# Kernel tuning notes

Measured on AMD Instinct MI355X. Metric: run time of the kernel, lower is better.

## Reference

```python
import jax, jax.numpy as jnp
import numpy as np

N, C = 65536, 1000

def setup_inputs() -> dict:
    key = jax.random.key(0)
    k1, k2 = jax.random.split(key)
    inp = jax.random.normal(k1, (N, C), dtype=jnp.float32)
    tgt = jax.random.randint(k2, (N,), 0, C, dtype=jnp.int64)
    return {"input": inp, "target": tgt}

def reference(input, target):
    # sign mask: +1 at the target class, -1 elsewhere (replaces the scatter loop)
    one_hot = jnp.arange(input.shape[1])[None, :] == target[:, None]  # [N, C] bool
    m = jnp.where(one_hot, input, -input)
    # piecewise huber-hinge: if m >= -1 -> max(0, 1-m)^2 else -4*m
    hinge = jnp.maximum(0.0, 1.0 - m)
    loss = jnp.where(m >= -1.0, hinge * hinge, -4.0 * m)
    return jnp.sum(loss) / target.shape[0]
```

## Files before the change

kernel.cpp:

```cpp
#include <hip/hip_runtime.h>


typedef float f4 __attribute__((ext_vector_type(4)));

constexpr int N_ROWS = 65536;
constexpr int N_COLS = 1000;
constexpr int F4_PER_ROW = N_COLS / 4;
constexpr int TOTAL_F4 = N_ROWS * F4_PER_ROW;

constexpr int BLOCK = 256;
constexpr int MAIN_GRID = 2000;
constexpr int CORR_GRID = 64;
constexpr int STRIDE_F4 = MAIN_GRID * BLOCK;
constexpr int ITERS = TOTAL_F4 / STRIDE_F4;
constexpr int BATCH = 8;

__device__ __forceinline__ float huber_f(float h) {
    float hc = fmaxf(fminf(h, 2.0f), 0.0f);
    return hc * fmaf(h, 2.0f, -hc);
}

__global__ __launch_bounds__(BLOCK) void mhl_kernel(const f4* __restrict__ in,
                                                    const float* __restrict__ in_f,
                                                    const int* __restrict__ tgt,
                                                    float* __restrict__ out) {
    float acc = 0.0f;

    if (blockIdx.x < CORR_GRID) {
        int tid = blockIdx.x * BLOCK + threadIdx.x;
#pragma unroll
        for (int k = 0; k < 4; ++k) {
            int r = tid + k * (CORR_GRID * BLOCK);
            int t = tgt[r];
            float x = in_f[r * N_COLS + t];
            acc += huber_f(1.0f - x) - huber_f(1.0f + x);
        }
    } else {
        int idx = (blockIdx.x - CORR_GRID) * BLOCK + threadIdx.x;
        int p = idx;
#pragma unroll 1
        for (int it = 0; it < ITERS / BATCH; ++it) {
            f4 v[BATCH];
#pragma unroll
            for (int j = 0; j < BATCH; ++j)
                v[j] = in[p + j * STRIDE_F4];
#pragma unroll
            for (int j = 0; j < BATCH; ++j) {
#pragma unroll
                for (int e = 0; e < 4; ++e) {
                    float h = 1.0f + v[j][e];
                    float hc = fmaxf(fminf(h, 2.0f), 0.0f);
                    acc = fmaf(hc, fmaf(h, 2.0f, -hc), acc);
                }
            }
            p += BATCH * STRIDE_F4;
        }
    }

#pragma unroll
    for (int off = 32; off > 0; off >>= 1)
        acc += __shfl_down(acc, off, 64);

    __shared__ float wsum[BLOCK / 64];
    int wid = threadIdx.x >> 6;
    int lane = threadIdx.x & 63;
    if (lane == 0) wsum[wid] = acc;
    __syncthreads();

    if (threadIdx.x == 0) {
        float s = wsum[0] + wsum[1] + wsum[2] + wsum[3];
        atomicAdd(out, s * (1.0f / (float)N_ROWS));
    }
}

extern "C" void kernel_launch(void* const* d_in, const int* in_sizes, int n_in,
                              void* d_out, int out_size, void* d_ws, size_t ws_size,
                              hipStream_t stream) {
    const f4* in = (const f4*)d_in[0];
    const float* in_f = (const float*)d_in[0];
    const int* tgt = (const int*)d_in[1];
    float* out = (float*)d_out;

    (void)hipMemsetAsync(out, 0, sizeof(float), stream);

    mhl_kernel<<<MAIN_GRID + CORR_GRID, BLOCK, 0, stream>>>(in, in_f, tgt, out);
}
```

Measured before the change: 58.66 us.

## Fold target-correction into main blocks and replace atomics with two-pass reduction

Removes the separate correction blocks: each of the 2000 streaming blocks now also handles 33 rows' target-class correction using its first threads. The global atomicAdd plus memset is replaced by per-block partial sums written to workspace, followed by a single-block reduce kernel. This drops the memset launch and atomic contention, but adds a second kernel launch and a dependency on the workspace buffer.

New measurement: 47.40 us. 1.24x faster.

```diff
diff --git a/kernel.cpp b/kernel.cpp
--- a/kernel.cpp
+++ b/kernel.cpp
@@ -9,52 +9,49 @@
 constexpr int TOTAL_F4 = N_ROWS * F4_PER_ROW;
 
 constexpr int BLOCK = 256;
-constexpr int MAIN_GRID = 2000;
-constexpr int CORR_GRID = 64;
-constexpr int STRIDE_F4 = MAIN_GRID * BLOCK;
+constexpr int GRID = 2000;
+constexpr int STRIDE_F4 = GRID * BLOCK;
 constexpr int ITERS = TOTAL_F4 / STRIDE_F4;
 constexpr int BATCH = 8;
+constexpr int ROWS_PER_BLOCK = 33;
 
 __device__ __forceinline__ float huber_f(float h) {
     float hc = fmaxf(fminf(h, 2.0f), 0.0f);
     return hc * fmaf(h, 2.0f, -hc);
 }
 
-__global__ __launch_bounds__(BLOCK) void mhl_kernel(const f4* __restrict__ in,
-                                                    const float* __restrict__ in_f,
-                                                    const int* __restrict__ tgt,
-                                                    float* __restrict__ out) {
+__global__ __launch_bounds__(BLOCK) void mhl_main(const f4* __restrict__ in,
+                                                  const float* __restrict__ in_f,
+                                                  const int* __restrict__ tgt,
+                                                  float* __restrict__ partial) {
     float acc = 0.0f;
 
-    if (blockIdx.x < CORR_GRID) {
-        int tid = blockIdx.x * BLOCK + threadIdx.x;
-#pragma unroll
-        for (int k = 0; k < 4; ++k) {
-            int r = tid + k * (CORR_GRID * BLOCK);
+    if (threadIdx.x < ROWS_PER_BLOCK) {
+        int r = blockIdx.x * ROWS_PER_BLOCK + threadIdx.x;
+        if (r < N_ROWS) {
             int t = tgt[r];
             float x = in_f[r * N_COLS + t];
             acc += huber_f(1.0f - x) - huber_f(1.0f + x);
         }
-    } else {
-        int idx = (blockIdx.x - CORR_GRID) * BLOCK + threadIdx.x;
-        int p = idx;
+    }
+
+    int p = blockIdx.x * BLOCK + threadIdx.x;
 #pragma unroll 1
-        for (int it = 0; it < ITERS / BATCH; ++it) {
-            f4 v[BATCH];
+    for (int it = 0; it < ITERS / BATCH; ++it) {
+        f4 v[BATCH];
 #pragma unroll
-            for (int j = 0; j < BATCH; ++j)
-                v[j] = in[p + j * STRIDE_F4];
+        for (int j = 0; j < BATCH; ++j)
+            v[j] = in[p + j * STRIDE_F4];
 #pragma unroll
-            for (int j = 0; j < BATCH; ++j) {
+        for (int j = 0; j < BATCH; ++j) {
 #pragma unroll
-                for (int e = 0; e < 4; ++e) {
-                    float h = 1.0f + v[j][e];
-                    float hc = fmaxf(fminf(h, 2.0f), 0.0f);
-                    acc = fmaf(hc, fmaf(h, 2.0f, -hc), acc);
-                }
+            for (int e = 0; e < 4; ++e) {
+                float h = 1.0f + v[j][e];
+                float hc = fmaxf(fminf(h, 2.0f), 0.0f);
+                acc = fmaf(hc, fmaf(h, 2.0f, -hc), acc);
             }
-            p += BATCH * STRIDE_F4;
         }
+        p += BATCH * STRIDE_F4;
     }
 
 #pragma unroll
@@ -62,15 +59,25 @@
         acc += __shfl_down(acc, off, 64);
 
     __shared__ float wsum[BLOCK / 64];
-    int wid = threadIdx.x >> 6;
-    int lane = threadIdx.x & 63;
-    if (lane == 0) wsum[wid] = acc;
+    if ((threadIdx.x & 63) == 0) wsum[threadIdx.x >> 6] = acc;
     __syncthreads();
+    if (threadIdx.x == 0)
+        partial[blockIdx.x] = wsum[0] + wsum[1] + wsum[2] + wsum[3];
+}
 
-    if (threadIdx.x == 0) {
-        float s = wsum[0] + wsum[1] + wsum[2] + wsum[3];
-        atomicAdd(out, s * (1.0f / (float)N_ROWS));
-    }
+__global__ __launch_bounds__(BLOCK) void mhl_reduce(const float* __restrict__ partial,
+                                                    float* __restrict__ out) {
+    float acc = 0.0f;
+    for (int i = threadIdx.x; i < GRID; i += BLOCK)
+        acc += partial[i];
+#pragma unroll
+    for (int off = 32; off > 0; off >>= 1)
+        acc += __shfl_down(acc, off, 64);
+    __shared__ float wsum[BLOCK / 64];
+    if ((threadIdx.x & 63) == 0) wsum[threadIdx.x >> 6] = acc;
+    __syncthreads();
+    if (threadIdx.x == 0)
+        out[0] = (wsum[0] + wsum[1] + wsum[2] + wsum[3]) * (1.0f / (float)N_ROWS);
 }
 
 extern "C" void kernel_launch(void* const* d_in, const int* in_sizes, int n_in,
@@ -80,8 +87,8 @@
     const float* in_f = (const float*)d_in[0];
     const int* tgt = (const int*)d_in[1];
     float* out = (float*)d_out;
+    float* partial = (float*)d_ws;
 
-    (void)hipMemsetAsync(out, 0, sizeof(float), stream);
-
-    mhl_kernel<<<MAIN_GRID + CORR_GRID, BLOCK, 0, stream>>>(in, in_f, tgt, out);
+    mhl_main<<<GRID, BLOCK, 0, stream>>>(in, in_f, tgt, partial);
+    mhl_reduce<<<1, BLOCK, 0, stream>>>(partial, out);
 }
```
